# Kernel tuning notes

Measured on AMD Instinct MI355X. Metric: run time of the kernel, lower is better.

The kernel has to match this reference:

```python
import jax, jax.numpy as jnp
import numpy as np

B, C, H, W = 32, 256, 64, 64
R = 16  # reduction
TOPK = 128


def setup_inputs() -> dict:
    key = jax.random.key(0)
    k_x, k_w1, k_b1, k_w2, k_b2 = jax.random.split(key, 5)
    return {
        "x": jax.random.normal(k_x, (B, C, H, W), dtype=jnp.float32),
        "w1": jax.random.normal(k_w1, (C // R, C), dtype=jnp.float32) * 0.05,
        "b1": jax.random.normal(k_b1, (C // R,), dtype=jnp.float32) * 0.05,
        "w2": jax.random.normal(k_w2, (C, C // R), dtype=jnp.float32) * 0.05,
        "b2": jax.random.normal(k_b2, (C,), dtype=jnp.float32) * 0.05,
        "topk": TOPK,
    }


def reference(x, w1, b1, w2, b2, topk):
    # Global average pool: [B, C, H, W] -> [B, C]
    y = jnp.mean(x, axis=(2, 3))
    # 1x1-conv squeeze-excite MLP (1x1 convs on a 1x1 spatial map == dense layers)
    h = jax.nn.relu(jnp.einsum("bc,rc->br", y, w1) + b1)
    attn_weight = jax.nn.sigmoid(jnp.einsum("br,cr->bc", h, w2) + b2)  # [B, C]
    # top-k channels by attention weight, then sort indices ascending
    _, idx = jax.lax.top_k(attn_weight, topk)          # [B, topk]
    idx = jnp.sort(idx, axis=1)
    # Fused: gather the selected channel weights and channels of x, multiply once
    aw_sel = jnp.take_along_axis(attn_weight, idx, axis=1)        # [B, topk]
    x_sel = jnp.take_along_axis(x, idx[:, :, None, None], axis=1)  # [B, topk, H, W]
    return aw_sel[:, :, None, None] * x_sel
```

## Files before the change

### kernel.cpp

```cpp
#include <hip/hip_runtime.h>

#define NB 32
#define NC 256
#define HW 4096
#define RDIM 16
#define KTOP 128

__global__ __launch_bounds__(256) void pool_kernel(const float* __restrict__ x,
                                                   float* __restrict__ y) {
    const int plane = blockIdx.x;
    const float4* __restrict__ xin =
        reinterpret_cast<const float4*>(x + (size_t)plane * HW);
    const int t = threadIdx.x;
    float s = 0.f;
#pragma unroll
    for (int i = 0; i < 4; ++i) {
        float4 v = xin[t + i * 256];
        s += (v.x + v.y) + (v.z + v.w);
    }
#pragma unroll
    for (int off = 32; off > 0; off >>= 1) s += __shfl_down(s, off);
    __shared__ float ws[4];
    const int wid = t >> 6, lane = t & 63;
    if (lane == 0) ws[wid] = s;
    __syncthreads();
    if (t == 0) {
        float tot = (ws[0] + ws[1]) + (ws[2] + ws[3]);
        y[plane] = tot * (1.0f / HW);
    }
}

__global__ __launch_bounds__(256) void se_topk_kernel(
    const float* __restrict__ y,
    const float* __restrict__ w1, const float* __restrict__ b1,
    const float* __restrict__ w2, const float* __restrict__ b2,
    int* __restrict__ idx_out, float* __restrict__ aw_out) {
    const int b = blockIdx.x;
    const int t = threadIdx.x;
    __shared__ float ych[NC];
    __shared__ float hsh[RDIM];
    __shared__ float attn[NC];
    __shared__ int   sel[NC];

    ych[t] = y[b * NC + t];
    __syncthreads();

    const int r = t >> 4;
    const int j = t & 15;
    float partial = 0.f;
#pragma unroll
    for (int k = 0; k < 16; ++k) {
        const int c = j * 16 + k;
        partial += ych[c] * w1[r * NC + c];
    }
#pragma unroll
    for (int m = 8; m > 0; m >>= 1) partial += __shfl_xor(partial, m, 16);
    if (j == 0) hsh[r] = fmaxf(partial + b1[r], 0.f);
    __syncthreads();

    float z = b2[t];
#pragma unroll
    for (int rr = 0; rr < RDIM; ++rr) z += hsh[rr] * w2[t * RDIM + rr];
    const float v = 1.0f / (1.0f + __expf(-z));
    attn[t] = v;
    __syncthreads();

    int rank = 0;
    for (int c = 0; c < NC; ++c) {
        const float o = attn[c];
        rank += (o > v) || (o == v && c < t);
    }
    const int s = (rank < KTOP) ? 1 : 0;
    sel[t] = s;
    __syncthreads();

    if (s) {
        int pos = 0;
        for (int c = 0; c < t; ++c) pos += sel[c];
        idx_out[b * KTOP + pos] = t;
        aw_out[b * KTOP + pos] = v;
    }
}

__global__ __launch_bounds__(256) void gather_scale_kernel(
    const float* __restrict__ x,
    const int* __restrict__ idx, const float* __restrict__ aw,
    float* __restrict__ out) {
    const int p = blockIdx.x;
    const int b = p >> 7;
    const int c = idx[p];
    const float w = aw[p];
    const float4* __restrict__ xin =
        reinterpret_cast<const float4*>(x + ((size_t)(b * NC + c)) * HW);
    float4* __restrict__ o = reinterpret_cast<float4*>(out + (size_t)p * HW);
    const int t = threadIdx.x;
#pragma unroll
    for (int i = 0; i < 4; ++i) {
        float4 vv = xin[t + i * 256];
        o[t + i * 256] = make_float4(w * vv.x, w * vv.y, w * vv.z, w * vv.w);
    }
}

extern "C" void kernel_launch(void* const* d_in, const int* in_sizes, int n_in,
                              void* d_out, int out_size, void* d_ws, size_t ws_size,
                              hipStream_t stream) {
    const float* x  = (const float*)d_in[0];
    const float* w1 = (const float*)d_in[1];
    const float* b1 = (const float*)d_in[2];
    const float* w2 = (const float*)d_in[3];
    const float* b2 = (const float*)d_in[4];
    float* out = (float*)d_out;

    float* y   = (float*)d_ws;
    int*   idx = (int*)(y + NB * NC);
    float* aw  = (float*)(idx + NB * KTOP);

    pool_kernel<<<NB * NC, 256, 0, stream>>>(x, y);
    se_topk_kernel<<<NB, 256, 0, stream>>>(y, w1, b1, w2, b2, idx, aw);
    gather_scale_kernel<<<NB * KTOP, 256, 0, stream>>>(x, idx, aw, out);
}
```

Before: 55.35 us.

## Map one wavefront per plane, use ballot prefix-sum, nontemporal output stores

Pool and gather kernels now give each 64-lane wavefront a whole 4096-element plane, so four planes share a block. This removes the shared-memory cross-wave reduction and __syncthreads in pooling and cuts the grid size by four. The top-k compaction swaps the serial shared-memory prefix scan for a wave ballot with popcount. Output stores in the gather use nontemporal hints to avoid polluting cache. Each lane now issues 16 loads instead of 4, which raises per-thread work and may reduce memory-level parallelism per wave.

New measurement: 55.10 us. Within noise of the previous version (-0.4%).

```diff
diff --git a/kernel.cpp b/kernel.cpp
--- a/kernel.cpp
+++ b/kernel.cpp
@@ -6,28 +6,23 @@
 #define RDIM 16
 #define KTOP 128
 
+typedef float v4f __attribute__((ext_vector_type(4)));
+
 __global__ __launch_bounds__(256) void pool_kernel(const float* __restrict__ x,
                                                    float* __restrict__ y) {
-    const int plane = blockIdx.x;
-    const float4* __restrict__ xin =
-        reinterpret_cast<const float4*>(x + (size_t)plane * HW);
-    const int t = threadIdx.x;
+    const int wid  = threadIdx.x >> 6;
+    const int lane = threadIdx.x & 63;
+    const int plane = blockIdx.x * 4 + wid;
+    const v4f* __restrict__ xin = (const v4f*)(x + (size_t)plane * HW);
     float s = 0.f;
 #pragma unroll
-    for (int i = 0; i < 4; ++i) {
-        float4 v = xin[t + i * 256];
+    for (int i = 0; i < 16; ++i) {
+        v4f v = xin[lane + i * 64];
         s += (v.x + v.y) + (v.z + v.w);
     }
 #pragma unroll
     for (int off = 32; off > 0; off >>= 1) s += __shfl_down(s, off);
-    __shared__ float ws[4];
-    const int wid = t >> 6, lane = t & 63;
-    if (lane == 0) ws[wid] = s;
-    __syncthreads();
-    if (t == 0) {
-        float tot = (ws[0] + ws[1]) + (ws[2] + ws[3]);
-        y[plane] = tot * (1.0f / HW);
-    }
+    if (lane == 0) y[plane] = s * (1.0f / HW);
 }
 
 __global__ __launch_bounds__(256) void se_topk_kernel(
@@ -37,10 +32,11 @@
     int* __restrict__ idx_out, float* __restrict__ aw_out) {
     const int b = blockIdx.x;
     const int t = threadIdx.x;
+    const int wid = t >> 6, lane = t & 63;
     __shared__ float ych[NC];
     __shared__ float hsh[RDIM];
     __shared__ float attn[NC];
-    __shared__ int   sel[NC];
+    __shared__ unsigned long long masks[4];
 
     ych[t] = y[b * NC + t];
     __syncthreads();
@@ -66,17 +62,20 @@
     __syncthreads();
 
     int rank = 0;
+#pragma unroll 4
     for (int c = 0; c < NC; ++c) {
         const float o = attn[c];
         rank += (o > v) || (o == v && c < t);
     }
-    const int s = (rank < KTOP) ? 1 : 0;
-    sel[t] = s;
+    const bool s = (rank < KTOP);
+
+    const unsigned long long m = __ballot(s);
+    if (lane == 0) masks[wid] = m;
     __syncthreads();
-
     if (s) {
-        int pos = 0;
-        for (int c = 0; c < t; ++c) pos += sel[c];
+        int pos = __popcll(m & ((lane == 63) ? 0x7FFFFFFFFFFFFFFFull
+                                             : ((1ull << lane) - 1ull)));
+        for (int w = 0; w < 4; ++w) pos += (w < wid) ? __popcll(masks[w]) : 0;
         idx_out[b * KTOP + pos] = t;
         aw_out[b * KTOP + pos] = v;
     }
@@ -86,18 +85,20 @@
     const float* __restrict__ x,
     const int* __restrict__ idx, const float* __restrict__ aw,
     float* __restrict__ out) {
-    const int p = blockIdx.x;
+    const int wid  = threadIdx.x >> 6;
+    const int lane = threadIdx.x & 63;
+    const int p = blockIdx.x * 4 + wid;
     const int b = p >> 7;
     const int c = idx[p];
     const float w = aw[p];
-    const float4* __restrict__ xin =
-        reinterpret_cast<const float4*>(x + ((size_t)(b * NC + c)) * HW);
-    float4* __restrict__ o = reinterpret_cast<float4*>(out + (size_t)p * HW);
-    const int t = threadIdx.x;
+    const v4f* __restrict__ xin =
+        (const v4f*)(x + ((size_t)b * NC + c) * HW);
+    v4f* __restrict__ o = (v4f*)(out + (size_t)p * HW);
 #pragma unroll
-    for (int i = 0; i < 4; ++i) {
-        float4 vv = xin[t + i * 256];
-        o[t + i * 256] = make_float4(w * vv.x, w * vv.y, w * vv.z, w * vv.w);
+    for (int i = 0; i < 16; ++i) {
+        v4f v = xin[lane + i * 64];
+        v4f rr = v * w;
+        __builtin_nontemporal_store(rr, &o[lane + i * 64]);
     }
 }
 
@@ -115,7 +116,7 @@
     int*   idx = (int*)(y + NB * NC);
     float* aw  = (float*)(idx + NB * KTOP);
 
-    pool_kernel<<<NB * NC, 256, 0, stream>>>(x, y);
+    pool_kernel<<<NB * NC / 4, 256, 0, stream>>>(x, y);
     se_topk_kernel<<<NB, 256, 0, stream>>>(y, w1, b1, w2, b2, idx, aw);
-    gather_scale_kernel<<<NB * KTOP, 256, 0, stream>>>(x, idx, aw, out);
+    gather_scale_kernel<<<NB * KTOP / 4, 256, 0, stream>>>(x, idx, aw, out);
 }
```
